# Kernel optimization log

Hardware: AMD Instinct MI355X
Metric: run time of the kernel (lower is better)

The kernel has to match this reference:

```python
import jax, jax.numpy as jnp
import numpy as np

D_MODEL = 1024
N_HEADS = 16
D_K = D_MODEL // N_HEADS


def setup_inputs() -> dict:
    key = jax.random.key(0)
    ks = jax.random.split(key, 12)
    B, S = 2, 2048
    scale = 1.0 / np.sqrt(D_MODEL)
    inp = {
        "q": jax.random.normal(ks[0], (B, S, D_MODEL), jnp.float32),
        "k": jax.random.normal(ks[1], (B, S, D_MODEL), jnp.float32),
        "v": jax.random.normal(ks[2], (B, S, D_MODEL), jnp.float32),
        "k_pe": jax.random.normal(ks[3], (N_HEADS, D_K, S), jnp.float32),
        "Wq": jax.random.normal(ks[4], (D_MODEL, D_MODEL), jnp.float32) * scale,
        "bq": jnp.zeros((D_MODEL,), jnp.float32),
        "Wk": jax.random.normal(ks[5], (D_MODEL, D_MODEL), jnp.float32) * scale,
        "bk": jnp.zeros((D_MODEL,), jnp.float32),
        "Wv": jax.random.normal(ks[6], (D_MODEL, D_MODEL), jnp.float32) * scale,
        "bv": jnp.zeros((D_MODEL,), jnp.float32),
        "Wo": jax.random.normal(ks[7], (D_MODEL, D_MODEL), jnp.float32) * scale,
        "bo": jnp.zeros((D_MODEL,), jnp.float32),
    }
    return inp


def reference(q, k, v, k_pe, Wq, bq, Wk, bk, Wv, bv, Wo, bo):
    B, S, _ = q.shape
    # projections -> [B, H, S, d_k]
    def split_heads(x):
        return x.reshape(B, S, N_HEADS, D_K).transpose(0, 2, 1, 3)
    qh = split_heads(q @ Wq + bq)
    kh = split_heads(k @ Wk + bk)
    vh = split_heads(v @ Wv + bv)
    # content scores + relative positional scores (two matmuls, summed)
    scores = jnp.einsum("bhsd,bhtd->bhst", qh, kh)
    scores = scores + jnp.einsum("bhsd,hdt->bhst", qh, k_pe)
    scores = scores / jnp.sqrt(jnp.asarray(D_K, qh.dtype))
    attn = jax.nn.softmax(scores, axis=-1)
    out = jnp.einsum("bhst,bhtd->bhsd", attn, vh)  # [B,H,S,d_k]
    out = out.transpose(0, 2, 1, 3).reshape(B, S, D_MODEL)
    return out @ Wo + bo
```

## Files before the change

kernel.cpp:

```cpp
#include <hip/hip_runtime.h>
#include <stdint.h>
#include <math.h>

typedef __bf16 bf16;
typedef __attribute__((ext_vector_type(8))) __bf16 bf16x8;
typedef __attribute__((ext_vector_type(4))) __bf16 bf16x4;
typedef __attribute__((ext_vector_type(4))) float f32x4;

#define MFMA_BF16(a, b, c) __builtin_amdgcn_mfma_f32_16x16x32_bf16((a), (b), (c), 0, 0, 0)

#if __has_builtin(__builtin_amdgcn_exp2f)
#define EXP2F __builtin_amdgcn_exp2f
#else
#define EXP2F exp2f
#endif

#define QSCALE 0.18033688011112042f

__device__ __forceinline__ void gl_lds16(const bf16* g, bf16* l) {
  __builtin_amdgcn_global_load_lds(
      (__attribute__((address_space(1))) unsigned int*)(uintptr_t)(g),
      (__attribute__((address_space(3))) unsigned int*)(l),
      16, 0, 0);
}

__global__ __launch_bounds__(256) void prep(
    const float* __restrict__ q, const float* __restrict__ k,
    const float* __restrict__ v, bf16* __restrict__ qb,
    bf16* __restrict__ kb, bf16* __restrict__ vb,
    const float* __restrict__ W0, const float* __restrict__ W1,
    const float* __restrict__ W2, const float* __restrict__ W3,
    bf16* __restrict__ Wt)
{
  __shared__ float tile[64][65];
  const int tid = threadIdx.x;
  const int bid = blockIdx.x;
  if (bid < 6144) {
    const int z = bid >> 11;
    const int idx = bid & 2047;
    const float* s = (z == 0) ? q : (z == 1) ? k : v;
    bf16* d = (z == 0) ? qb : (z == 1) ? kb : vb;
    size_t i = ((size_t)idx * 256 + tid) * 8;
    float4 a = *(const float4*)(s + i);
    float4 b = *(const float4*)(s + i + 4);
    bf16x8 o;
    o[0] = (bf16)a.x; o[1] = (bf16)a.y; o[2] = (bf16)a.z; o[3] = (bf16)a.w;
    o[4] = (bf16)b.x; o[5] = (bf16)b.y; o[6] = (bf16)b.z; o[7] = (bf16)b.w;
    *(bf16x8*)(d + i) = o;
  } else {
    const int t = bid - 6144;
    const int z = t >> 8;
    const int rem = t & 255;
    const int r0 = (rem >> 4) * 64, c0 = (rem & 15) * 64;
    const float* src = (z == 0) ? W0 : (z == 1) ? W1 : (z == 2) ? W2 : W3;
    bf16* dst = Wt + (size_t)z * (1024 * 1024);
#pragma unroll
    for (int h = 0; h < 2; ++h) {
      int qq = tid + h * 256;
      int row = qq >> 3, cc = qq & 7;
      float4 a = *(const float4*)(src + (size_t)(r0 + row) * 1024 + c0 + cc * 8);
      float4 b = *(const float4*)(src + (size_t)(r0 + row) * 1024 + c0 + cc * 8 + 4);
      tile[row][cc * 8 + 0] = a.x; tile[row][cc * 8 + 1] = a.y;
      tile[row][cc * 8 + 2] = a.z; tile[row][cc * 8 + 3] = a.w;
      tile[row][cc * 8 + 4] = b.x; tile[row][cc * 8 + 5] = b.y;
      tile[row][cc * 8 + 6] = b.z; tile[row][cc * 8 + 7] = b.w;
    }
    __syncthreads();
#pragma unroll
    for (int h = 0; h < 2; ++h) {
      int qq = tid + h * 256;
      int row = qq >> 3, cc = qq & 7;
      bf16x8 o;
#pragma unroll
      for (int e = 0; e < 8; ++e) o[e] = (bf16)tile[cc * 8 + e][row];
      *(bf16x8*)(dst + (size_t)(c0 + row) * 1024 + r0 + cc * 8) = o;
    }
  }
}

template <int MODE>
__device__ __forceinline__ void gemm_body(
    const bf16* __restrict__ A, const bf16* __restrict__ Wt,
    const float* __restrict__ bias, float oscale, void* __restrict__ out_v)
{
  __shared__ __align__(16) bf16 As[128 * 32];
  __shared__ __align__(16) bf16 Bs[128 * 32];
  const int tid = threadIdx.x;
  const int w = tid >> 6, lane = tid & 63;
  const int lm = lane & 15, quad = lane >> 4;
  const int wr = w >> 1, wc = w & 1;
  const int m0 = blockIdx.y * 128, n0 = blockIdx.x * 128;

  f32x4 zero4 = {0.f, 0.f, 0.f, 0.f};
  f32x4 acc[4][4];
#pragma unroll
  for (int i = 0; i < 4; ++i)
#pragma unroll
    for (int j = 0; j < 4; ++j) acc[i][j] = zero4;

  for (int kb = 0; kb < 32; ++kb) {
    __syncthreads();
#pragma unroll
    for (int h = 0; h < 2; ++h) {
      int qq = tid + h * 256;
      int row = qq >> 2, cs = qq & 3;
      int cc = cs ^ ((row >> 1) & 3);
      gl_lds16(A + (size_t)(m0 + row) * 1024 + kb * 32 + cc * 8, As + qq * 8);
      gl_lds16(Wt + (size_t)(n0 + row) * 1024 + kb * 32 + cc * 8, Bs + qq * 8);
    }
    __syncthreads();

    bf16x8 af[4], bfv[4];
#pragma unroll
    for (int i = 0; i < 4; ++i) {
      int row = wr * 64 + i * 16 + lm;
      af[i] = *(const bf16x8*)(As + row * 32 + ((quad ^ ((row >> 1) & 3)) * 8));
    }
#pragma unroll
    for (int j = 0; j < 4; ++j) {
      int row = wc * 64 + j * 16 + lm;
      bfv[j] = *(const bf16x8*)(Bs + row * 32 + ((quad ^ ((row >> 1) & 3)) * 8));
    }
#pragma unroll
    for (int i = 0; i < 4; ++i)
#pragma unroll
      for (int j = 0; j < 4; ++j)
        acc[i][j] = MFMA_BF16(af[i], bfv[j], acc[i][j]);
  }

  const int ncol = n0 + wc * 64;
  float bv4[4];
#pragma unroll
  for (int j = 0; j < 4; ++j) bv4[j] = bias[ncol + j * 16 + lm];
#pragma unroll
  for (int i = 0; i < 4; ++i) {
#pragma unroll
    for (int j = 0; j < 4; ++j) {
      const int ng = ncol + j * 16 + lm;
      const int hh = ng >> 6, d = ng & 63;
#pragma unroll
      for (int r = 0; r < 4; ++r) {
        const int mg = m0 + wr * 64 + i * 16 + quad * 4 + r;
        const int b = mg >> 11, s = mg & 2047;
        float val = acc[i][j][r] + bv4[j];
        if (MODE == 0) {
          ((bf16*)out_v)[(((size_t)(b * 16 + hh)) * 2048 + s) * 64 + d] =
              (bf16)(val * oscale);
        } else {
          ((float*)out_v)[(size_t)mg * 1024 + ng] = val;
        }
      }
    }
  }
}

__global__ __launch_bounds__(256) void qkv_gemm(
    const bf16* __restrict__ qb, const bf16* __restrict__ kb, const bf16* __restrict__ vb,
    const bf16* __restrict__ Wt, const float* __restrict__ biq,
    const float* __restrict__ bik, const float* __restrict__ biv,
    bf16* __restrict__ Qs, bf16* __restrict__ Ks, bf16* __restrict__ Vrow)
{
  const int z = blockIdx.z;
  if (z == 0) {
    gemm_body<0>(qb, Wt, biq, QSCALE, Qs);
  } else if (z == 1) {
    gemm_body<0>(kb, Wt + (size_t)1 * 1024 * 1024, bik, 1.f, Ks);
  } else {
    gemm_body<0>(vb, Wt + (size_t)2 * 1024 * 1024, biv, 1.f, Vrow);
  }
}

__global__ __launch_bounds__(256) void out_gemm(
    const bf16* __restrict__ A, const bf16* __restrict__ Wt,
    const float* __restrict__ bias, float* __restrict__ out)
{
  gemm_body<3>(A, Wt, bias, 1.f, out);
}

__global__ __launch_bounds__(256) void post_kv(
    const float* __restrict__ kpe, bf16* __restrict__ Ks,
    const bf16* __restrict__ Vrow, bf16* __restrict__ Vts)
{
  const int tid = threadIdx.x;
  const int bh = blockIdx.y;
  const int t0 = blockIdx.x * 64;
  if (blockIdx.z == 0) {
    __shared__ float tile[64][65];
    const int h = bh & 15;
    const float* src = kpe + (size_t)h * 64 * 2048;
#pragma unroll
    for (int p = 0; p < 2; ++p) {
      int qq = tid + p * 256;
      int d = qq >> 3, cs = qq & 7;
      float4 a = *(const float4*)(src + (size_t)d * 2048 + t0 + cs * 8);
      float4 b = *(const float4*)(src + (size_t)d * 2048 + t0 + cs * 8 + 4);
      tile[d][cs * 8 + 0] = a.x; tile[d][cs * 8 + 1] = a.y;
      tile[d][cs * 8 + 2] = a.z; tile[d][cs * 8 + 3] = a.w;
      tile[d][cs * 8 + 4] = b.x; tile[d][cs * 8 + 5] = b.y;
      tile[d][cs * 8 + 6] = b.z; tile[d][cs * 8 + 7] = b.w;
    }
    __syncthreads();
    bf16* krow = Ks + (size_t)bh * 2048 * 64;
#pragma unroll
    for (int p = 0; p < 2; ++p) {
      int qq = tid + p * 256;
      int t = qq >> 3, cs = qq & 7;
      bf16x8 kv = *(const bf16x8*)(krow + (size_t)(t0 + t) * 64 + cs * 8);
      bf16x8 o;
#pragma unroll
      for (int e = 0; e < 8; ++e) o[e] = (bf16)((float)kv[e] + tile[cs * 8 + e][t]);
      *(bf16x8*)(krow + (size_t)(t0 + t) * 64 + cs * 8) = o;
    }
  } else {
    __shared__ bf16 btile[64][72];
    const bf16* src = Vrow + (size_t)bh * 2048 * 64;
#pragma unroll
    for (int p = 0; p < 2; ++p) {
      int qq = tid + p * 256;
      int t = qq >> 3, cs = qq & 7;
      *(bf16x8*)(&btile[t][cs * 8]) =
          *(const bf16x8*)(src + (size_t)(t0 + t) * 64 + cs * 8);
    }
    __syncthreads();
    bf16* dst = Vts + (size_t)bh * 64 * 2048;
#pragma unroll
    for (int p = 0; p < 2; ++p) {
      int qq = tid + p * 256;
      int d = qq >> 3, cs = qq & 7;
      bf16x8 o;
#pragma unroll
      for (int e = 0; e < 8; ++e) o[e] = btile[cs * 8 + e][d];
      *(bf16x8*)(dst + (size_t)d * 2048 + t0 + cs * 8) = o;
    }
  }
}

__global__ __launch_bounds__(512) void flash_attn(
    const bf16* __restrict__ Q, const bf16* __restrict__ K,
    const bf16* __restrict__ Vt, bf16* __restrict__ O)
{
  __shared__ __align__(16) bf16 Qt[128 * 64];
  __shared__ __align__(16) bf16 Kt[64 * 64];
  __shared__ __align__(16) bf16 Vs[64 * 64];
  __shared__ __align__(16) bf16 Ps[128 * 72];

  const int tid = threadIdx.x;
  const int w = tid >> 6, lane = tid & 63;
  const int lm = lane & 15, quad = lane >> 4;
  const int bh = blockIdx.y;
  const int s0 = blockIdx.x * 128;
  const size_t qkbase = (size_t)bh * (2048 * 64);
  const size_t vbase = (size_t)bh * (64 * 2048);

#pragma unroll
  for (int h = 0; h < 2; ++h) {
    int qq = tid + h * 512;
    int row = qq >> 3, cs = qq & 7;
    int cc = cs ^ (row & 7);
    gl_lds16(Q + qkbase + (size_t)(s0 + row) * 64 + cc * 8, Qt + qq * 8);
  }
  __syncthreads();

  bf16x8 qa0, qa1;
  {
    int row = w * 16 + lm;
    qa0 = *(const bf16x8*)(Qt + row * 64 + ((quad ^ (row & 7)) * 8));
    qa1 = *(const bf16x8*)(Qt + row * 64 + (((quad + 4) ^ (row & 7)) * 8));
  }

  f32x4 zero4 = {0.f, 0.f, 0.f, 0.f};
  float l_part = 0.f;
  f32x4 oacc[4];
#pragma unroll
  for (int dt = 0; dt < 4; ++dt) oacc[dt] = zero4;

  const int prow = (w * 16 + lm) * 72;

  for (int kt = 0; kt < 32; ++kt) {
    const int t0 = kt * 64;
    __syncthreads();
    {
      int row = tid >> 3, cs = tid & 7;
      int cc = cs ^ (row & 7);
      gl_lds16(K + qkbase + (size_t)(t0 + row) * 64 + cc * 8, Kt + tid * 8);
      gl_lds16(Vt + vbase + (size_t)row * 2048 + t0 + cc * 8, Vs + tid * 8);
    }
    __syncthreads();

#pragma unroll
    for (int c = 0; c < 4; ++c) {
      int row = c * 16 + lm;
      bf16x8 kb0 = *(const bf16x8*)(Kt + row * 64 + ((quad ^ (row & 7)) * 8));
      bf16x8 kb1 = *(const bf16x8*)(Kt + row * 64 + (((quad + 4) ^ (row & 7)) * 8));
      f32x4 z = MFMA_BF16(kb0, qa0, zero4);
      f32x4 st = MFMA_BF16(kb1, qa1, z);
      bf16x4 pk;
#pragma unroll
      for (int r = 0; r < 4; ++r) {
        float p = EXP2F(st[r]);
        l_part += p;
        pk[r] = (bf16)p;
      }
      *(bf16x4*)(Ps + prow + c * 16 + quad * 4) = pk;
    }

    bf16x8 pa0 = *(const bf16x8*)(Ps + prow + quad * 8);
    bf16x8 pa1 = *(const bf16x8*)(Ps + prow + 32 + quad * 8);
#pragma unroll
    for (int dt = 0; dt < 4; ++dt) {
      int row = dt * 16 + lm;
      bf16x8 va0 = *(const bf16x8*)(Vs + row * 64 + ((quad ^ (row & 7)) * 8));
      bf16x8 va1 = *(const bf16x8*)(Vs + row * 64 + (((quad + 4) ^ (row & 7)) * 8));
      oacc[dt] = MFMA_BF16(va0, pa0, oacc[dt]);
      oacc[dt] = MFMA_BF16(va1, pa1, oacc[dt]);
    }
  }

  float l = l_part;
  l += __shfl_xor(l, 16, 64);
  l += __shfl_xor(l, 32, 64);
  float inv = 1.f / l;
#pragma unroll
  for (int dt = 0; dt < 4; ++dt)
#pragma unroll
    for (int r = 0; r < 4; ++r)
      Ps[prow + dt * 16 + quad * 4 + r] = (bf16)(oacc[dt][r] * inv);

  const int b = bh >> 4, hh = bh & 15;
  const int srow = s0 + w * 16 + lm;
  const size_t ob = ((size_t)(b * 2048 + srow)) * 1024 + hh * 64;
#pragma unroll
  for (int half = 0; half < 2; ++half) {
    bf16x8 ov = *(const bf16x8*)(Ps + prow + (half * 4 + quad) * 8);
    *(bf16x8*)(O + ob + (half * 4 + quad) * 8) = ov;
  }
}

extern "C" void kernel_launch(void* const* d_in, const int* in_sizes, int n_in,
                              void* d_out, int out_size, void* d_ws, size_t ws_size,
                              hipStream_t stream) {
  (void)in_sizes; (void)n_in; (void)out_size; (void)ws_size;
  const float* q   = (const float*)d_in[0];
  const float* k   = (const float*)d_in[1];
  const float* v   = (const float*)d_in[2];
  const float* kpe = (const float*)d_in[3];
  const float* Wq  = (const float*)d_in[4];
  const float* bq  = (const float*)d_in[5];
  const float* Wk  = (const float*)d_in[6];
  const float* bk  = (const float*)d_in[7];
  const float* Wv  = (const float*)d_in[8];
  const float* bv  = (const float*)d_in[9];
  const float* Wo  = (const float*)d_in[10];
  const float* bo  = (const float*)d_in[11];

  const size_t NT = 4u * 1024 * 1024;
  bf16* ws  = (bf16*)d_ws;
  bf16* Wt  = ws;
  bf16* qb  = Wt + NT;
  bf16* kb  = qb + NT;
  bf16* vb  = kb + NT;
  bf16* Qs  = vb + NT;
  bf16* Ks  = Qs + NT;
  bf16* Vts = Ks + NT;
  bf16* Oa  = Vts + NT;
  bf16* Vrow = Oa;

  prep<<<dim3(7168), 256, 0, stream>>>(q, k, v, qb, kb, vb, Wq, Wk, Wv, Wo, Wt);
  qkv_gemm<<<dim3(8, 32, 3), 256, 0, stream>>>(qb, kb, vb, Wt, bq, bk, bv,
                                               Qs, Ks, Vrow);
  post_kv<<<dim3(32, 32, 2), 256, 0, stream>>>(kpe, Ks, Vrow, Vts);
  flash_attn<<<dim3(16, 32), 512, 0, stream>>>(Qs, Ks, Vts, Oa);
  out_gemm<<<dim3(8, 32), 256, 0, stream>>>(Oa, Wt + 3u * 1024 * 1024, bo,
                                            (float*)d_out);
}
```

Measured before the change: 241.8 us.

## Fuse k_pe add and V transpose into QKV GEMM epilogue; double-buffer attention K/V

The separate post_kv kernel is removed. Its k_pe addition now happens in the K projection epilogue, and the V projection epilogue writes V directly in transposed [d, t] layout. This drops one kernel launch and a full read/write round trip of K and V. The flash attention loop now double-buffers the K/V tiles and prefetches the next tile while computing the current one, using one barrier per iteration instead of two. The trade-offs are more LDS per block and strided or less coalesced epilogue stores, including bf16x4 column writes for V.

```diff
diff --git a/kernel.cpp b/kernel.cpp
--- a/kernel.cpp
+++ b/kernel.cpp
@@ -81,7 +81,8 @@
 template <int MODE>
 __device__ __forceinline__ void gemm_body(
     const bf16* __restrict__ A, const bf16* __restrict__ Wt,
-    const float* __restrict__ bias, float oscale, void* __restrict__ out_v)
+    const float* __restrict__ bias, float oscale,
+    const float* __restrict__ kpe, void* __restrict__ out_v)
 {
   __shared__ __align__(16) bf16 As[128 * 32];
   __shared__ __align__(16) bf16 Bs[128 * 32];
@@ -134,20 +135,38 @@
   for (int j = 0; j < 4; ++j) bv4[j] = bias[ncol + j * 16 + lm];
 #pragma unroll
   for (int i = 0; i < 4; ++i) {
+    const int mbase = m0 + wr * 64 + i * 16 + quad * 4;
+    const int b = mbase >> 11, s = mbase & 2047;
 #pragma unroll
     for (int j = 0; j < 4; ++j) {
       const int ng = ncol + j * 16 + lm;
       const int hh = ng >> 6, d = ng & 63;
-#pragma unroll
-      for (int r = 0; r < 4; ++r) {
-        const int mg = m0 + wr * 64 + i * 16 + quad * 4 + r;
-        const int b = mg >> 11, s = mg & 2047;
-        float val = acc[i][j][r] + bv4[j];
-        if (MODE == 0) {
-          ((bf16*)out_v)[(((size_t)(b * 16 + hh)) * 2048 + s) * 64 + d] =
+      if (MODE == 2) {
+        bf16x4 o;
+#pragma unroll
+        for (int r = 0; r < 4; ++r) o[r] = (bf16)(acc[i][j][r] + bv4[j]);
+        *(bf16x4*)((bf16*)out_v + ((size_t)(b * 16 + hh) * 64 + d) * 2048 + s) = o;
+      } else if (MODE == 1) {
+        float4 p4 = *(const float4*)(kpe + ((size_t)(hh * 64 + d)) * 2048 + s);
+        float pe[4] = {p4.x, p4.y, p4.z, p4.w};
+#pragma unroll
+        for (int r = 0; r < 4; ++r) {
+          float val = acc[i][j][r] + bv4[j] + pe[r];
+          ((bf16*)out_v)[(((size_t)(b * 16 + hh)) * 2048 + (s + r)) * 64 + d] =
+              (bf16)val;
+        }
+      } else if (MODE == 0) {
+#pragma unroll
+        for (int r = 0; r < 4; ++r) {
+          float val = acc[i][j][r] + bv4[j];
+          ((bf16*)out_v)[(((size_t)(b * 16 + hh)) * 2048 + (s + r)) * 64 + d] =
               (bf16)(val * oscale);
-        } else {
-          ((float*)out_v)[(size_t)mg * 1024 + ng] = val;
+        }
+      } else {
+#pragma unroll
+        for (int r = 0; r < 4; ++r) {
+          float val = acc[i][j][r] + bv4[j];
+          ((float*)out_v)[(size_t)(mbase + r) * 1024 + ng] = val;
         }
       }
     }
@@ -158,15 +177,16 @@
     const bf16* __restrict__ qb, const bf16* __restrict__ kb, const bf16* __restrict__ vb,
     const bf16* __restrict__ Wt, const float* __restrict__ biq,
     const float* __restrict__ bik, const float* __restrict__ biv,
-    bf16* __restrict__ Qs, bf16* __restrict__ Ks, bf16* __restrict__ Vrow)
+    const float* __restrict__ kpe,
+    bf16* __restrict__ Qs, bf16* __restrict__ Ks, bf16* __restrict__ Vts)
 {
   const int z = blockIdx.z;
   if (z == 0) {
-    gemm_body<0>(qb, Wt, biq, QSCALE, Qs);
+    gemm_body<0>(qb, Wt, biq, QSCALE, nullptr, Qs);
   } else if (z == 1) {
-    gemm_body<0>(kb, Wt + (size_t)1 * 1024 * 1024, bik, 1.f, Ks);
+    gemm_body<1>(kb, Wt + (size_t)1 * 1024 * 1024, bik, 1.f, kpe, Ks);
   } else {
-    gemm_body<0>(vb, Wt + (size_t)2 * 1024 * 1024, biv, 1.f, Vrow);
+    gemm_body<2>(vb, Wt + (size_t)2 * 1024 * 1024, biv, 1.f, nullptr, Vts);
   }
 }
 
@@ -174,65 +194,7 @@
     const bf16* __restrict__ A, const bf16* __restrict__ Wt,
     const float* __restrict__ bias, float* __restrict__ out)
 {
-  gemm_body<3>(A, Wt, bias, 1.f, out);
-}
-
-__global__ __launch_bounds__(256) void post_kv(
-    const float* __restrict__ kpe, bf16* __restrict__ Ks,
-    const bf16* __restrict__ Vrow, bf16* __restrict__ Vts)
-{
-  const int tid = threadIdx.x;
-  const int bh = blockIdx.y;
-  const int t0 = blockIdx.x * 64;
-  if (blockIdx.z == 0) {
-    __shared__ float tile[64][65];
-    const int h = bh & 15;
-    const float* src = kpe + (size_t)h * 64 * 2048;
-#pragma unroll
-    for (int p = 0; p < 2; ++p) {
-      int qq = tid + p * 256;
-      int d = qq >> 3, cs = qq & 7;
-      float4 a = *(const float4*)(src + (size_t)d * 2048 + t0 + cs * 8);
-      float4 b = *(const float4*)(src + (size_t)d * 2048 + t0 + cs * 8 + 4);
-      tile[d][cs * 8 + 0] = a.x; tile[d][cs * 8 + 1] = a.y;
-      tile[d][cs * 8 + 2] = a.z; tile[d][cs * 8 + 3] = a.w;
-      tile[d][cs * 8 + 4] = b.x; tile[d][cs * 8 + 5] = b.y;
-      tile[d][cs * 8 + 6] = b.z; tile[d][cs * 8 + 7] = b.w;
-    }
-    __syncthreads();
-    bf16* krow = Ks + (size_t)bh * 2048 * 64;
-#pragma unroll
-    for (int p = 0; p < 2; ++p) {
-      int qq = tid + p * 256;
-      int t = qq >> 3, cs = qq & 7;
-      bf16x8 kv = *(const bf16x8*)(krow + (size_t)(t0 + t) * 64 + cs * 8);
-      bf16x8 o;
-#pragma unroll
-      for (int e = 0; e < 8; ++e) o[e] = (bf16)((float)kv[e] + tile[cs * 8 + e][t]);
-      *(bf16x8*)(krow + (size_t)(t0 + t) * 64 + cs * 8) = o;
-    }
-  } else {
-    __shared__ bf16 btile[64][72];
-    const bf16* src = Vrow + (size_t)bh * 2048 * 64;
-#pragma unroll
-    for (int p = 0; p < 2; ++p) {
-      int qq = tid + p * 256;
-      int t = qq >> 3, cs = qq & 7;
-      *(bf16x8*)(&btile[t][cs * 8]) =
-          *(const bf16x8*)(src + (size_t)(t0 + t) * 64 + cs * 8);
-    }
-    __syncthreads();
-    bf16* dst = Vts + (size_t)bh * 64 * 2048;
-#pragma unroll
-    for (int p = 0; p < 2; ++p) {
-      int qq = tid + p * 256;
-      int d = qq >> 3, cs = qq & 7;
-      bf16x8 o;
-#pragma unroll
-      for (int e = 0; e < 8; ++e) o[e] = btile[cs * 8 + e][d];
-      *(bf16x8*)(dst + (size_t)d * 2048 + t0 + cs * 8) = o;
-    }
-  }
+  gemm_body<3>(A, Wt, bias, 1.f, nullptr, out);
 }
 
 __global__ __launch_bounds__(512) void flash_attn(
@@ -240,8 +202,8 @@
     const bf16* __restrict__ Vt, bf16* __restrict__ O)
 {
   __shared__ __align__(16) bf16 Qt[128 * 64];
-  __shared__ __align__(16) bf16 Kt[64 * 64];
-  __shared__ __align__(16) bf16 Vs[64 * 64];
+  __shared__ __align__(16) bf16 Kt[2][64 * 64];
+  __shared__ __align__(16) bf16 Vs[2][64 * 64];
   __shared__ __align__(16) bf16 Ps[128 * 72];
 
   const int tid = threadIdx.x;
@@ -259,6 +221,12 @@
     int cc = cs ^ (row & 7);
     gl_lds16(Q + qkbase + (size_t)(s0 + row) * 64 + cc * 8, Qt + qq * 8);
   }
+  {
+    int row = tid >> 3, cs = tid & 7;
+    int cc = cs ^ (row & 7);
+    gl_lds16(K + qkbase + (size_t)row * 64 + cc * 8, Kt[0] + tid * 8);
+    gl_lds16(Vt + vbase + (size_t)row * 2048 + cc * 8, Vs[0] + tid * 8);
+  }
   __syncthreads();
 
   bf16x8 qa0, qa1;
@@ -277,21 +245,20 @@
   const int prow = (w * 16 + lm) * 72;
 
   for (int kt = 0; kt < 32; ++kt) {
-    const int t0 = kt * 64;
-    __syncthreads();
-    {
+    const int cur = kt & 1;
+    if (kt < 31) {
+      const int t1 = (kt + 1) * 64;
       int row = tid >> 3, cs = tid & 7;
       int cc = cs ^ (row & 7);
-      gl_lds16(K + qkbase + (size_t)(t0 + row) * 64 + cc * 8, Kt + tid * 8);
-      gl_lds16(Vt + vbase + (size_t)row * 2048 + t0 + cc * 8, Vs + tid * 8);
-    }
-    __syncthreads();
+      gl_lds16(K + qkbase + (size_t)(t1 + row) * 64 + cc * 8, Kt[cur ^ 1] + tid * 8);
+      gl_lds16(Vt + vbase + (size_t)row * 2048 + t1 + cc * 8, Vs[cur ^ 1] + tid * 8);
+    }
 
 #pragma unroll
     for (int c = 0; c < 4; ++c) {
       int row = c * 16 + lm;
-      bf16x8 kb0 = *(const bf16x8*)(Kt + row * 64 + ((quad ^ (row & 7)) * 8));
-      bf16x8 kb1 = *(const bf16x8*)(Kt + row * 64 + (((quad + 4) ^ (row & 7)) * 8));
+      bf16x8 kb0 = *(const bf16x8*)(Kt[cur] + row * 64 + ((quad ^ (row & 7)) * 8));
+      bf16x8 kb1 = *(const bf16x8*)(Kt[cur] + row * 64 + (((quad + 4) ^ (row & 7)) * 8));
       f32x4 z = MFMA_BF16(kb0, qa0, zero4);
       f32x4 st = MFMA_BF16(kb1, qa1, z);
       bf16x4 pk;
@@ -309,11 +276,13 @@
 #pragma unroll
     for (int dt = 0; dt < 4; ++dt) {
       int row = dt * 16 + lm;
-      bf16x8 va0 = *(const bf16x8*)(Vs + row * 64 + ((quad ^ (row & 7)) * 8));
-      bf16x8 va1 = *(const bf16x8*)(Vs + row * 64 + (((quad + 4) ^ (row & 7)) * 8));
+      bf16x8 va0 = *(const bf16x8*)(Vs[cur] + row * 64 + ((quad ^ (row & 7)) * 8));
+      bf16x8 va1 = *(const bf16x8*)(Vs[cur] + row * 64 + (((quad + 4) ^ (row & 7)) * 8));
       oacc[dt] = MFMA_BF16(va0, pa0, oacc[dt]);
       oacc[dt] = MFMA_BF16(va1, pa1, oacc[dt]);
     }
+
+    __syncthreads();
   }
 
   float l = l_part;
@@ -363,12 +332,10 @@
   bf16* Ks  = Qs + NT;
   bf16* Vts = Ks + NT;
   bf16* Oa  = Vts + NT;
-  bf16* Vrow = Oa;
 
   prep<<<dim3(7168), 256, 0, stream>>>(q, k, v, qb, kb, vb, Wq, Wk, Wv, Wo, Wt);
-  qkv_gemm<<<dim3(8, 32, 3), 256, 0, stream>>>(qb, kb, vb, Wt, bq, bk, bv,
-                                               Qs, Ks, Vrow);
-  post_kv<<<dim3(32, 32, 2), 256, 0, stream>>>(kpe, Ks, Vrow, Vts);
+  qkv_gemm<<<dim3(8, 32, 3), 256, 0, stream>>>(qb, kb, vb, Wt, bq, bk, bv, kpe,
+                                               Qs, Ks, Vts);
   flash_attn<<<dim3(16, 32), 512, 0, stream>>>(Qs, Ks, Vts, Oa);
   out_gemm<<<dim3(8, 32), 256, 0, stream>>>(Oa, Wt + 3u * 1024 * 1024, bo,
                                             (float*)d_out);
```

Measured after the change: 248.2 us. +2.6%, slower.
